# Performance work log

Hardware: AMD Instinct MI355X
Metric: run time of the kernel (lower is better)

## Reference

```python
import jax, jax.numpy as jnp
import numpy as np

E = 16   # stroke embedding dim
H = 2    # attention heads
HD = E // H

def setup_inputs() -> dict:
    key = jax.random.key(0)
    ks = jax.random.split(key, 16)
    N, L, B = 100000, 8, 200000
    node_features = jax.random.normal(ks[0], (N, 6), dtype=jnp.float32)
    stroke_to_loop = jax.random.randint(ks[1], (B, L), 0, N, dtype=jnp.int64)
    def lin(k, o, i):
        bound = 1.0 / np.sqrt(i)
        kw, kb = jax.random.split(k)
        w = jax.random.uniform(kw, (o, i), jnp.float32, -bound, bound)
        b = jax.random.uniform(kb, (o,), jnp.float32, -bound, bound)
        return w, b
    fc1_w, fc1_b = lin(ks[2], 32, 6)
    fc2_w, fc2_b = lin(ks[3], E, 32)
    in_proj_w, in_proj_b = lin(ks[4], 3 * E, E)
    out_proj_w, out_proj_b = lin(ks[5], E, E)
    fc_w, fc_b = lin(ks[6], 32, E)
    fco_w, fco_b = lin(ks[7], 32, 32)
    return {"node_features": node_features, "stroke_to_loop": stroke_to_loop,
            "fc1_w": fc1_w, "fc1_b": fc1_b, "fc2_w": fc2_w, "fc2_b": fc2_b,
            "in_proj_w": in_proj_w, "in_proj_b": in_proj_b,
            "out_proj_w": out_proj_w, "out_proj_b": out_proj_b,
            "fc_w": fc_w, "fc_b": fc_b, "fco_w": fco_w, "fco_b": fco_b}

def reference(node_features, stroke_to_loop, fc1_w, fc1_b, fc2_w, fc2_b,
              in_proj_w, in_proj_b, out_proj_w, out_proj_b,
              fc_w, fc_b, fco_w, fco_b):
    B, L = stroke_to_loop.shape
    # per-loop gather: [B, L, 6]
    strokes = node_features[stroke_to_loop]
    # stroke MLP: 6 -> 32 -> 16
    h = jax.nn.relu(jnp.einsum('bli,oi->blo', strokes, fc1_w) + fc1_b)
    x = jnp.einsum('bli,oi->blo', h, fc2_w) + fc2_b  # [B, L, E]
    # multihead self-attention (embed_dim=16, heads=2)
    qkv = jnp.einsum('ble,oe->blo', x, in_proj_w) + in_proj_b  # [B, L, 3E]
    q, k, v = jnp.split(qkv, 3, axis=-1)
    q = q.reshape(B, L, H, HD)
    k = k.reshape(B, L, H, HD)
    v = v.reshape(B, L, H, HD)
    scores = jnp.einsum('blhd,bmhd->bhlm', q, k) / np.sqrt(HD).astype(np.float32)
    attn = jax.nn.softmax(scores, axis=-1)
    ctx = jnp.einsum('bhlm,bmhd->blhd', attn, v).reshape(B, L, E)
    attn_out = jnp.einsum('ble,oe->blo', ctx, out_proj_w) + out_proj_b
    # fc -> relu -> mean over strokes -> fc_output
    y = jax.nn.relu(jnp.einsum('ble,oe->blo', attn_out, fc_w) + fc_b)
    y = y.mean(axis=1)  # [B, 32]
    return jnp.einsum('bi,oi->bo', y, fco_w) + fco_b
```

## Files before the change

kernel.cpp:

```cpp
#include <hip/hip_runtime.h>


typedef float f32x4 __attribute__((ext_vector_type(4)));
typedef __fp16 h2 __attribute__((ext_vector_type(2)));

static __device__ __forceinline__ unsigned h2u(h2 v) { return __builtin_bit_cast(unsigned, v); }
static __device__ __forceinline__ h2 u2h(unsigned v) { return __builtin_bit_cast(h2, v); }
static __device__ __forceinline__ h2 f2h(float v) { return __builtin_bit_cast(h2, v); }
static __device__ __forceinline__ float h2f(h2 v) { return __builtin_bit_cast(float, v); }
#define DPPH2(x, ctrl) u2h((unsigned)__builtin_amdgcn_update_dpp( \
    (int)h2u(x), (int)h2u(x), (ctrl), 0xF, 0xF, false))
#define SWZH(x, pat) u2h((unsigned)__builtin_amdgcn_ds_swizzle((int)h2u(x), (pat)))

#if defined(__has_builtin) && __has_builtin(__builtin_amdgcn_fdot2)
#define FDOT2(a, b, c) __builtin_amdgcn_fdot2((a), (b), (c), false)
#else
#define FDOT2(a, b, c) fmaf((float)(a).x, (float)(b).x, fmaf((float)(a).y, (float)(b).y, (c)))
#endif

#if defined(__has_builtin) && __has_builtin(__builtin_elementwise_fma)
#define PKFMA(a, b, c) __builtin_elementwise_fma((a), (b), (c))
#else
#define PKFMA(a, b, c) ((a) * (b) + (c))
#endif

__global__ __launch_bounds__(256) void prep_kernel(
    const float* __restrict__ nf,
    const float* __restrict__ w1, const float* __restrict__ b1,
    const float* __restrict__ w2, const float* __restrict__ b2,
    const float* __restrict__ wip, const float* __restrict__ bip,
    const float* __restrict__ fcw, const float* __restrict__ fcb,
    const float* __restrict__ opw, const float* __restrict__ opb,
    const float* __restrict__ fow,
    float* __restrict__ qkvt, h2* __restrict__ w3h,
    h2* __restrict__ fowh, float* __restrict__ b3, float* __restrict__ w3f,
    int N)
{
    if ((int)blockIdx.x == (int)gridDim.x - 1) {
        __shared__ float lw[512];
        int t = threadIdx.x;
#pragma unroll
        for (int rep = 0; rep < 2; ++rep) {
            int id = t + rep * 256;
            int o = id >> 4, j = id & 15;
            float acc = 0.f;
#pragma unroll
            for (int e = 0; e < 16; ++e)
                acc = fmaf(fcw[o * 16 + e], opw[e * 16 + j], acc);
            lw[id] = acc;
        }
        if (t < 32) {
            float bb = fcb[t];
#pragma unroll
            for (int e = 0; e < 16; ++e) bb = fmaf(fcw[t * 16 + e], opb[e], bb);
            b3[t] = bb;
        }
        fowh[t]       = __builtin_amdgcn_cvt_pkrtz(fow[2 * t],       fow[2 * t + 1]);
        fowh[t + 256] = __builtin_amdgcn_cvt_pkrtz(fow[2 * t + 512], fow[2 * t + 513]);
        __syncthreads();
        w3h[t] = __builtin_amdgcn_cvt_pkrtz(lw[2 * t], lw[2 * t + 1]);
        w3f[t] = lw[t];
        w3f[t + 256] = lw[t + 256];
        return;
    }
    int n = blockIdx.x * 256 + threadIdx.x;
    if (n >= N) return;
    const float2* nfp = reinterpret_cast<const float2*>(nf);
    float2 p0 = nfp[n * 3 + 0], p1 = nfp[n * 3 + 1], p2 = nfp[n * 3 + 2];
    float f[6] = {p0.x, p0.y, p1.x, p1.y, p2.x, p2.y};
    float h[32];
#pragma unroll
    for (int o = 0; o < 32; ++o) {
        float acc = b1[o];
#pragma unroll
        for (int i = 0; i < 6; ++i) acc = fmaf(f[i], w1[o * 6 + i], acc);
        h[o] = fmaxf(acc, 0.f);
    }
    float x[16];
#pragma unroll
    for (int e = 0; e < 16; ++e) {
        float acc = b2[e];
#pragma unroll
        for (int i = 0; i < 32; ++i) acc = fmaf(h[i], w2[e * 32 + i], acc);
        x[e] = acc;
    }
    float qkv[48];
#pragma unroll
    for (int c = 0; c < 48; ++c) {
        float acc = bip[c];
#pragma unroll
        for (int e = 0; e < 16; ++e) acc = fmaf(x[e], wip[c * 16 + e], acc);
        qkv[c] = acc;
    }
    const float cs = 0.35355339059327373f * 1.4426950408889634f;
#pragma unroll
    for (int c = 0; c < 16; ++c) qkv[c] *= cs;
    h2 ph[24];
#pragma unroll
    for (int i = 0; i < 24; ++i)
        ph[i] = __builtin_amdgcn_cvt_pkrtz(qkv[2 * i], qkv[2 * i + 1]);
    f32x4* dst = reinterpret_cast<f32x4*>(qkvt) + (size_t)n * 6;
#pragma unroll
    for (int t2 = 0; t2 < 6; ++t2) {
        f32x4 w;
        w.x = h2f(ph[4 * t2 + 0]); w.y = h2f(ph[4 * t2 + 1]);
        w.z = h2f(ph[4 * t2 + 2]); w.w = h2f(ph[4 * t2 + 3]);
        dst[t2] = w;
    }
}

__global__ __launch_bounds__(256) void attn_tail_kernel(
    const int* __restrict__ s2l, const float* __restrict__ qkvt,
    const h2* __restrict__ w3h, const float* __restrict__ b3,
    const h2* __restrict__ fowh, const float* __restrict__ fob,
    float* __restrict__ out, int B)
{
    int tid = blockIdx.x * 256 + threadIdx.x;
    int l = tid & 7;
    int g = tid >> 3;
    int npair = (B + 1) >> 1;
    if (g >= npair) return;
    int b0 = 2 * g, b1 = 2 * g + 1;
    bool have1 = (b1 < B);
    int idx0 = s2l[b0 * 8 + l];
    int idx1 = s2l[(have1 ? b1 : b0) * 8 + l];
    const f32x4* qp0 = reinterpret_cast<const f32x4*>(qkvt) + (size_t)idx0 * 6;
    const f32x4* qp1 = reinterpret_cast<const f32x4*>(qkvt) + (size_t)idx1 * 6;

    f32x4 x0 = qp0[0], x1 = qp0[1], x2 = qp0[2], x3 = qp0[3], x4 = qp0[4], x5 = qp0[5];
    f32x4 y0 = qp1[0], y1 = qp1[1], y2 = qp1[2], y3 = qp1[3], y4 = qp1[4], y5 = qp1[5];

    h2 qh[2][8], kh[2][8], vh[2][8];
    qh[0][0]=f2h(x0.x); qh[0][1]=f2h(x0.y); qh[0][2]=f2h(x0.z); qh[0][3]=f2h(x0.w);
    qh[0][4]=f2h(x1.x); qh[0][5]=f2h(x1.y); qh[0][6]=f2h(x1.z); qh[0][7]=f2h(x1.w);
    kh[0][0]=f2h(x2.x); kh[0][1]=f2h(x2.y); kh[0][2]=f2h(x2.z); kh[0][3]=f2h(x2.w);
    kh[0][4]=f2h(x3.x); kh[0][5]=f2h(x3.y); kh[0][6]=f2h(x3.z); kh[0][7]=f2h(x3.w);
    vh[0][0]=f2h(x4.x); vh[0][1]=f2h(x4.y); vh[0][2]=f2h(x4.z); vh[0][3]=f2h(x4.w);
    vh[0][4]=f2h(x5.x); vh[0][5]=f2h(x5.y); vh[0][6]=f2h(x5.z); vh[0][7]=f2h(x5.w);
    qh[1][0]=f2h(y0.x); qh[1][1]=f2h(y0.y); qh[1][2]=f2h(y0.z); qh[1][3]=f2h(y0.w);
    qh[1][4]=f2h(y1.x); qh[1][5]=f2h(y1.y); qh[1][6]=f2h(y1.z); qh[1][7]=f2h(y1.w);
    kh[1][0]=f2h(y2.x); kh[1][1]=f2h(y2.y); kh[1][2]=f2h(y2.z); kh[1][3]=f2h(y2.w);
    kh[1][4]=f2h(y3.x); kh[1][5]=f2h(y3.y); kh[1][6]=f2h(y3.z); kh[1][7]=f2h(y3.w);
    vh[1][0]=f2h(y4.x); vh[1][1]=f2h(y4.y); vh[1][2]=f2h(y4.z); vh[1][3]=f2h(y4.w);
    vh[1][4]=f2h(y5.x); vh[1][5]=f2h(y5.y); vh[1][6]=f2h(y5.z); vh[1][7]=f2h(y5.w);

    h2 k7[2][8];
#pragma unroll
    for (int d = 0; d < 8; ++d) {
        k7[0][d] = DPPH2(kh[0][d], 0x141);
        k7[1][d] = DPPH2(kh[1][d], 0x141);
    }

    float s0[2][8], s1[2][8];
#define SC_ID(i, slot, KS) { float u0 = 0.f, u1 = 0.f; \
    _Pragma("unroll") for (int d = 0; d < 4; ++d) { \
        u0 = FDOT2(qh[i][d], KS[i][d], u0); \
        u1 = FDOT2(qh[i][4 + d], KS[i][4 + d], u1); } \
    s0[i][slot] = u0; s1[i][slot] = u1; }
#define SC_DPP(i, slot, KS, CTRL) { float u0 = 0.f, u1 = 0.f; \
    _Pragma("unroll") for (int d = 0; d < 4; ++d) { \
        u0 = FDOT2(qh[i][d], DPPH2(KS[i][d], CTRL), u0); \
        u1 = FDOT2(qh[i][4 + d], DPPH2(KS[i][4 + d], CTRL), u1); } \
    s0[i][slot] = u0; s1[i][slot] = u1; }
    SC_ID(0, 0, kh)          SC_ID(1, 0, kh)
    SC_DPP(0, 1, kh, 0xB1)   SC_DPP(1, 1, kh, 0xB1)
    SC_DPP(0, 2, kh, 0x4E)   SC_DPP(1, 2, kh, 0x4E)
    SC_DPP(0, 3, kh, 0x1B)   SC_DPP(1, 3, kh, 0x1B)
    SC_DPP(0, 4, k7, 0x1B)   SC_DPP(1, 4, k7, 0x1B)
    SC_DPP(0, 5, k7, 0x4E)   SC_DPP(1, 5, k7, 0x4E)
    SC_DPP(0, 6, k7, 0xB1)   SC_DPP(1, 6, k7, 0xB1)
    SC_ID(0, 7, k7)          SC_ID(1, 7, k7)
#undef SC_ID
#undef SC_DPP

    h2 eA[2][8], eB[2][8];
#pragma unroll
    for (int i = 0; i < 2; ++i) {
        float e0[8], e1[8];
        float sum0 = 0.f, sum1 = 0.f;
#pragma unroll
        for (int m = 0; m < 8; ++m) {
            e0[m] = exp2f(s0[i][m]); sum0 += e0[m];
            e1[m] = exp2f(s1[i][m]); sum1 += e1[m];
        }
        float r0 = __builtin_amdgcn_rcpf(sum0);
        float r1 = __builtin_amdgcn_rcpf(sum1);
#pragma unroll
        for (int m = 0; m < 8; ++m) {
            float n0 = e0[m] * r0, n1 = e1[m] * r1;
            eA[i][m] = __builtin_amdgcn_cvt_pkrtz(n0, n0);
            eB[i][m] = __builtin_amdgcn_cvt_pkrtz(n1, n1);
        }
    }

    h2 v7[2][8];
#pragma unroll
    for (int d = 0; d < 8; ++d) {
        v7[0][d] = DPPH2(vh[0][d], 0x141);
        v7[1][d] = DPPH2(vh[1][d], 0x141);
    }

    h2 cx[2][8];
    h2 hz; hz.x = (__fp16)0.f; hz.y = (__fp16)0.f;
#pragma unroll
    for (int i = 0; i < 2; ++i)
#pragma unroll
        for (int d = 0; d < 8; ++d) cx[i][d] = hz;
#define CTX_ID(i, slot, VS) { \
    _Pragma("unroll") for (int d = 0; d < 4; ++d) { \
        cx[i][d]     = PKFMA(eA[i][slot], VS[i][d],     cx[i][d]); \
        cx[i][4 + d] = PKFMA(eB[i][slot], VS[i][4 + d], cx[i][4 + d]); } }
#define CTX_DPP(i, slot, VS, CTRL) { \
    _Pragma("unroll") for (int d = 0; d < 4; ++d) { \
        cx[i][d]     = PKFMA(eA[i][slot], DPPH2(VS[i][d], CTRL),     cx[i][d]); \
        cx[i][4 + d] = PKFMA(eB[i][slot], DPPH2(VS[i][4 + d], CTRL), cx[i][4 + d]); } }
    CTX_ID(0, 0, vh)          CTX_ID(1, 0, vh)
    CTX_DPP(0, 1, vh, 0xB1)   CTX_DPP(1, 1, vh, 0xB1)
    CTX_DPP(0, 2, vh, 0x4E)   CTX_DPP(1, 2, vh, 0x4E)
    CTX_DPP(0, 3, vh, 0x1B)   CTX_DPP(1, 3, vh, 0x1B)
    CTX_DPP(0, 4, v7, 0x1B)   CTX_DPP(1, 4, v7, 0x1B)
    CTX_DPP(0, 5, v7, 0x4E)   CTX_DPP(1, 5, v7, 0x4E)
    CTX_DPP(0, 6, v7, 0xB1)   CTX_DPP(1, 6, v7, 0xB1)
    CTX_ID(0, 7, v7)          CTX_ID(1, 7, v7)
#undef CTX_ID
#undef CTX_DPP

    h2 yh[2][16];
#pragma unroll
    for (int i = 0; i < 16; ++i) {
        float ba = b3[2 * i], bb = b3[2 * i + 1];
        float ya0 = ba, yb0 = bb, ya1 = ba, yb1 = bb;
#pragma unroll
        for (int jj = 0; jj < 8; ++jj) {
            h2 wa = w3h[(2 * i) * 8 + jj];
            h2 wb = w3h[(2 * i + 1) * 8 + jj];
            ya0 = FDOT2(cx[0][jj], wa, ya0);
            ya1 = FDOT2(cx[1][jj], wa, ya1);
            yb0 = FDOT2(cx[0][jj], wb, yb0);
            yb1 = FDOT2(cx[1][jj], wb, yb1);
        }
        yh[0][i] = __builtin_amdgcn_cvt_pkrtz(fmaxf(ya0, 0.f), fmaxf(yb0, 0.f));
        yh[1][i] = __builtin_amdgcn_cvt_pkrtz(fmaxf(ya1, 0.f), fmaxf(yb1, 0.f));
    }

#pragma unroll
    for (int i = 0; i < 16; ++i) {
#pragma unroll
        for (int j = 0; j < 2; ++j) {
            yh[j][i] = yh[j][i] + SWZH(yh[j][i], 0x041F);
            yh[j][i] = yh[j][i] + SWZH(yh[j][i], 0x081F);
            yh[j][i] = yh[j][i] + SWZH(yh[j][i], 0x101F);
        }
    }

    float o4a[4], o4b[4];
#pragma unroll
    for (int j = 0; j < 4; ++j) {
        int oo = l * 4 + j;
        float acc0 = 0.f, acc1 = 0.f;
#pragma unroll
        for (int i = 0; i < 16; ++i) {
            h2 w = fowh[oo * 16 + i];
            acc0 = FDOT2(yh[0][i], w, acc0);
            acc1 = FDOT2(yh[1][i], w, acc1);
        }
        float bo = fob[oo];
        o4a[j] = fmaf(acc0, 0.125f, bo);
        o4b[j] = fmaf(acc1, 0.125f, bo);
    }
    f32x4 res0; res0.x = o4a[0]; res0.y = o4a[1]; res0.z = o4a[2]; res0.w = o4a[3];
    __builtin_nontemporal_store(res0, reinterpret_cast<f32x4*>(out) + (b0 * 8 + l));
    if (have1) {
        f32x4 res1; res1.x = o4b[0]; res1.y = o4b[1]; res1.z = o4b[2]; res1.w = o4b[3];
        __builtin_nontemporal_store(res1, reinterpret_cast<f32x4*>(out) + (b1 * 8 + l));
    }
}

__global__ __launch_bounds__(256) void loop_embed_kernel(
    const float* __restrict__ nf, const int* __restrict__ s2l,
    const float* __restrict__ w1, const float* __restrict__ b1,
    const float* __restrict__ w2, const float* __restrict__ b2,
    const float* __restrict__ wip, const float* __restrict__ bip,
    const float* __restrict__ w3, const float* __restrict__ b3,
    const float* __restrict__ fow, const float* __restrict__ fob,
    float* __restrict__ out, int B)
{
    int tid = blockIdx.x * 256 + threadIdx.x;
    int b = tid >> 3;
    if (b >= B) return;
    int l = tid & 7;
    int idx = s2l[b * 8 + l];
    const float2* nfp = reinterpret_cast<const float2*>(nf);
    float2 p0 = nfp[idx * 3 + 0], p1 = nfp[idx * 3 + 1], p2 = nfp[idx * 3 + 2];
    float f[6] = {p0.x, p0.y, p1.x, p1.y, p2.x, p2.y};
    float h[32];
#pragma unroll
    for (int o = 0; o < 32; ++o) {
        float acc = b1[o];
#pragma unroll
        for (int i = 0; i < 6; ++i) acc = fmaf(f[i], w1[o * 6 + i], acc);
        h[o] = fmaxf(acc, 0.f);
    }
    float x[16];
#pragma unroll
    for (int e = 0; e < 16; ++e) {
        float acc = b2[e];
#pragma unroll
        for (int i = 0; i < 32; ++i) acc = fmaf(h[i], w2[e * 32 + i], acc);
        x[e] = acc;
    }
    float q[16], k[16], v[16];
#pragma unroll
    for (int c = 0; c < 16; ++c) {
        float aq = bip[c], ak = bip[16 + c], av = bip[32 + c];
#pragma unroll
        for (int e = 0; e < 16; ++e) {
            aq = fmaf(x[e], wip[c * 16 + e], aq);
            ak = fmaf(x[e], wip[(16 + c) * 16 + e], ak);
            av = fmaf(x[e], wip[(32 + c) * 16 + e], av);
        }
        q[c] = aq; k[c] = ak; v[c] = av;
    }
    int lane = threadIdx.x & 63;
    int gb = lane & 56;
    float s0[8], s1[8];
#pragma unroll
    for (int m = 0; m < 8; ++m) {
        float a0 = 0.f, a1 = 0.f;
#pragma unroll
        for (int d = 0; d < 8; ++d) {
            a0 = fmaf(q[d], __shfl(k[d], gb + m, 64), a0);
            a1 = fmaf(q[8 + d], __shfl(k[8 + d], gb + m, 64), a1);
        }
        s0[m] = a0; s1[m] = a1;
    }
    const float sc = 0.35355339059327373f;
    float mx0 = s0[0], mx1 = s1[0];
#pragma unroll
    for (int m = 1; m < 8; ++m) { mx0 = fmaxf(mx0, s0[m]); mx1 = fmaxf(mx1, s1[m]); }
    float e0[8], e1[8];
    float sum0 = 0.f, sum1 = 0.f;
#pragma unroll
    for (int m = 0; m < 8; ++m) {
        e0[m] = __expf((s0[m] - mx0) * sc); sum0 += e0[m];
        e1[m] = __expf((s1[m] - mx1) * sc); sum1 += e1[m];
    }
    float r0 = 1.0f / sum0, r1 = 1.0f / sum1;
    float ctx[16];
#pragma unroll
    for (int c = 0; c < 16; ++c) ctx[c] = 0.f;
#pragma unroll
    for (int m = 0; m < 8; ++m) {
#pragma unroll
        for (int c = 0; c < 8; ++c)
            ctx[c] = fmaf(e0[m], __shfl(v[c], gb + m, 64), ctx[c]);
#pragma unroll
        for (int c = 8; c < 16; ++c)
            ctx[c] = fmaf(e1[m], __shfl(v[c], gb + m, 64), ctx[c]);
    }
#pragma unroll
    for (int c = 0; c < 8; ++c)  ctx[c] *= r0;
#pragma unroll
    for (int c = 8; c < 16; ++c) ctx[c] *= r1;
    float y[32];
#pragma unroll
    for (int o = 0; o < 32; ++o) {
        float acc = b3[o];
#pragma unroll
        for (int j = 0; j < 16; ++j) acc = fmaf(ctx[j], w3[o * 16 + j], acc);
        y[o] = fmaxf(acc, 0.f);
    }
#pragma unroll
    for (int o = 0; o < 32; ++o) {
        y[o] += __shfl_xor(y[o], 1, 64);
        y[o] += __shfl_xor(y[o], 2, 64);
        y[o] += __shfl_xor(y[o], 4, 64);
    }
    float o4[4];
#pragma unroll
    for (int j = 0; j < 4; ++j) {
        int oo = l * 4 + j;
        float acc = 0.f;
#pragma unroll
        for (int i = 0; i < 32; ++i) acc = fmaf(y[i], fow[oo * 32 + i], acc);
        o4[j] = fmaf(acc, 0.125f, fob[oo]);
    }
    reinterpret_cast<float4*>(out)[b * 8 + l] = make_float4(o4[0], o4[1], o4[2], o4[3]);
}

extern "C" void kernel_launch(void* const* d_in, const int* in_sizes, int n_in,
                              void* d_out, int out_size, void* d_ws, size_t ws_size,
                              hipStream_t stream) {
    const float* nf  = (const float*)d_in[0];
    const int*   s2l = (const int*)d_in[1];
    const float* w1  = (const float*)d_in[2];
    const float* b1  = (const float*)d_in[3];
    const float* w2  = (const float*)d_in[4];
    const float* b2  = (const float*)d_in[5];
    const float* wip = (const float*)d_in[6];
    const float* bip = (const float*)d_in[7];
    const float* opw = (const float*)d_in[8];
    const float* opb = (const float*)d_in[9];
    const float* fcw = (const float*)d_in[10];
    const float* fcb = (const float*)d_in[11];
    const float* fow = (const float*)d_in[12];
    const float* fob = (const float*)d_in[13];
    float* out = (float*)d_out;

    int N = in_sizes[0] / 6;
    int B = in_sizes[1] / 8;

    unsigned* wsd = (unsigned*)d_ws;
    h2*    w3h  = (h2*)(wsd);
    h2*    fowh = (h2*)(wsd + 256);
    float* b3   = (float*)(wsd + 768);
    float* w3f  = (float*)(wsd + 800);
    float* qkvt = (float*)(wsd + 1312);

    size_t need = (size_t)(1312 + (size_t)N * 12) * 4;

    if (ws_size >= need) {
        int NB = (N + 255) / 256;
        prep_kernel<<<NB + 1, 256, 0, stream>>>(
            nf, w1, b1, w2, b2, wip, bip, fcw, fcb, opw, opb, fow,
            qkvt, w3h, fowh, b3, w3f, N);
        int npair = (B + 1) >> 1;
        int threads = npair * 8;
        int blocks = (threads + 255) / 256;
        attn_tail_kernel<<<blocks, 256, 0, stream>>>(
            s2l, qkvt, w3h, b3, fowh, fob, out, B);
    } else {
        prep_kernel<<<1, 256, 0, stream>>>(
            nf, w1, b1, w2, b2, wip, bip, fcw, fcb, opw, opb, fow,
            qkvt, w3h, fowh, b3, w3f, 0);
        int blocks = (B * 8 + 255) / 256;
        loop_embed_kernel<<<blocks, 256, 0, stream>>>(
            nf, s2l, w1, b1, w2, b2, wip, bip, w3f, b3, fow, fob, out, B);
    }
    (void)n_in; (void)out_size;
}
```

Measured before the change: 83.07 us.

## Fuse prep and attention kernels into one cooperative persistent kernel with grid sync

Combines the per-node QKV precompute and the per-loop attention tail into one cooperative kernel. It uses grid-stride loops sized to occupancy and a grid-wide barrier between the two phases. This is meant to remove the second kernel launch and the gap between the kernels. In exchange it adds a grid sync and host-side occupancy queries on every call, and it gives up the larger oversubscribed grid. The old two-kernel path is kept as a fallback if the cooperative launch fails.

```diff
diff --git a/kernel.cpp b/kernel.cpp
--- a/kernel.cpp
+++ b/kernel.cpp
@@ -1,5 +1,8 @@
 #include <hip/hip_runtime.h>
-
+#include <hip/hip_cooperative_groups.h>
+
+
+namespace cg = cooperative_groups;
 
 typedef float f32x4 __attribute__((ext_vector_type(4)));
 typedef __fp16 h2 __attribute__((ext_vector_type(2)));
@@ -24,47 +27,14 @@
 #define PKFMA(a, b, c) ((a) * (b) + (c))
 #endif
 
-__global__ __launch_bounds__(256) void prep_kernel(
+
+static __device__ __forceinline__ void qkv_node_body(
     const float* __restrict__ nf,
     const float* __restrict__ w1, const float* __restrict__ b1,
     const float* __restrict__ w2, const float* __restrict__ b2,
     const float* __restrict__ wip, const float* __restrict__ bip,
-    const float* __restrict__ fcw, const float* __restrict__ fcb,
-    const float* __restrict__ opw, const float* __restrict__ opb,
-    const float* __restrict__ fow,
-    float* __restrict__ qkvt, h2* __restrict__ w3h,
-    h2* __restrict__ fowh, float* __restrict__ b3, float* __restrict__ w3f,
-    int N)
+    float* __restrict__ qkvt, int n)
 {
-    if ((int)blockIdx.x == (int)gridDim.x - 1) {
-        __shared__ float lw[512];
-        int t = threadIdx.x;
-#pragma unroll
-        for (int rep = 0; rep < 2; ++rep) {
-            int id = t + rep * 256;
-            int o = id >> 4, j = id & 15;
-            float acc = 0.f;
-#pragma unroll
-            for (int e = 0; e < 16; ++e)
-                acc = fmaf(fcw[o * 16 + e], opw[e * 16 + j], acc);
-            lw[id] = acc;
-        }
-        if (t < 32) {
-            float bb = fcb[t];
-#pragma unroll
-            for (int e = 0; e < 16; ++e) bb = fmaf(fcw[t * 16 + e], opb[e], bb);
-            b3[t] = bb;
-        }
-        fowh[t]       = __builtin_amdgcn_cvt_pkrtz(fow[2 * t],       fow[2 * t + 1]);
-        fowh[t + 256] = __builtin_amdgcn_cvt_pkrtz(fow[2 * t + 512], fow[2 * t + 513]);
-        __syncthreads();
-        w3h[t] = __builtin_amdgcn_cvt_pkrtz(lw[2 * t], lw[2 * t + 1]);
-        w3f[t] = lw[t];
-        w3f[t + 256] = lw[t + 256];
-        return;
-    }
-    int n = blockIdx.x * 256 + threadIdx.x;
-    if (n >= N) return;
     const float2* nfp = reinterpret_cast<const float2*>(nf);
     float2 p0 = nfp[n * 3 + 0], p1 = nfp[n * 3 + 1], p2 = nfp[n * 3 + 2];
     float f[6] = {p0.x, p0.y, p1.x, p1.y, p2.x, p2.y};
@@ -109,17 +79,14 @@
     }
 }
 
-__global__ __launch_bounds__(256) void attn_tail_kernel(
+static __device__ __forceinline__ void attn_pair_body(
     const int* __restrict__ s2l, const float* __restrict__ qkvt,
     const h2* __restrict__ w3h, const float* __restrict__ b3,
     const h2* __restrict__ fowh, const float* __restrict__ fob,
-    float* __restrict__ out, int B)
+    float* __restrict__ out, int B, int t)
 {
-    int tid = blockIdx.x * 256 + threadIdx.x;
-    int l = tid & 7;
-    int g = tid >> 3;
-    int npair = (B + 1) >> 1;
-    if (g >= npair) return;
+    int l = t & 7;
+    int g = t >> 3;
     int b0 = 2 * g, b1 = 2 * g + 1;
     bool have1 = (b1 < B);
     int idx0 = s2l[b0 * 8 + l];
@@ -276,6 +243,110 @@
     }
 }
 
+__global__ __launch_bounds__(256) void fused_kernel(
+    const float* __restrict__ nf,
+    const float* __restrict__ w1, const float* __restrict__ b1,
+    const float* __restrict__ w2, const float* __restrict__ b2,
+    const float* __restrict__ wip, const float* __restrict__ bip,
+    const float* __restrict__ fcw, const float* __restrict__ fcb,
+    const float* __restrict__ opw, const float* __restrict__ opb,
+    const float* __restrict__ fow, const float* __restrict__ fob,
+    const int* __restrict__ s2l,
+    float* __restrict__ qkvt, h2* __restrict__ w3h,
+    h2* __restrict__ fowh, float* __restrict__ b3w,
+    float* __restrict__ out, int N, int B)
+{
+    int t = threadIdx.x;
+    if (blockIdx.x == 0) {
+        __shared__ float lw[512];
+#pragma unroll
+        for (int rep = 0; rep < 2; ++rep) {
+            int id = t + rep * 256;
+            int o = id >> 4, j = id & 15;
+            float acc = 0.f;
+#pragma unroll
+            for (int e = 0; e < 16; ++e)
+                acc = fmaf(fcw[o * 16 + e], opw[e * 16 + j], acc);
+            lw[id] = acc;
+        }
+        if (t < 32) {
+            float bb = fcb[t];
+#pragma unroll
+            for (int e = 0; e < 16; ++e) bb = fmaf(fcw[t * 16 + e], opb[e], bb);
+            b3w[t] = bb;
+        }
+        fowh[t]       = __builtin_amdgcn_cvt_pkrtz(fow[2 * t],       fow[2 * t + 1]);
+        fowh[t + 256] = __builtin_amdgcn_cvt_pkrtz(fow[2 * t + 512], fow[2 * t + 513]);
+        __syncthreads();
+        w3h[t] = __builtin_amdgcn_cvt_pkrtz(lw[2 * t], lw[2 * t + 1]);
+    }
+    for (int n = blockIdx.x * 256 + t; n < N; n += gridDim.x * 256)
+        qkv_node_body(nf, w1, b1, w2, b2, wip, bip, qkvt, n);
+
+    cg::this_grid().sync();
+
+    int npair = (B + 1) >> 1;
+    int total = npair * 8;
+    for (int i = blockIdx.x * 256 + t; i < total; i += gridDim.x * 256)
+        attn_pair_body(s2l, qkvt, w3h, b3w, fowh, fob, out, B, i);
+}
+
+__global__ __launch_bounds__(256) void prep_kernel(
+    const float* __restrict__ nf,
+    const float* __restrict__ w1, const float* __restrict__ b1,
+    const float* __restrict__ w2, const float* __restrict__ b2,
+    const float* __restrict__ wip, const float* __restrict__ bip,
+    const float* __restrict__ fcw, const float* __restrict__ fcb,
+    const float* __restrict__ opw, const float* __restrict__ opb,
+    const float* __restrict__ fow,
+    float* __restrict__ qkvt, h2* __restrict__ w3h,
+    h2* __restrict__ fowh, float* __restrict__ b3, float* __restrict__ w3f,
+    int N)
+{
+    if ((int)blockIdx.x == (int)gridDim.x - 1) {
+        __shared__ float lw[512];
+        int t = threadIdx.x;
+#pragma unroll
+        for (int rep = 0; rep < 2; ++rep) {
+            int id = t + rep * 256;
+            int o = id >> 4, j = id & 15;
+            float acc = 0.f;
+#pragma unroll
+            for (int e = 0; e < 16; ++e)
+                acc = fmaf(fcw[o * 16 + e], opw[e * 16 + j], acc);
+            lw[id] = acc;
+        }
+        if (t < 32) {
+            float bb = fcb[t];
+#pragma unroll
+            for (int e = 0; e < 16; ++e) bb = fmaf(fcw[t * 16 + e], opb[e], bb);
+            b3[t] = bb;
+        }
+        fowh[t]       = __builtin_amdgcn_cvt_pkrtz(fow[2 * t],       fow[2 * t + 1]);
+        fowh[t + 256] = __builtin_amdgcn_cvt_pkrtz(fow[2 * t + 512], fow[2 * t + 513]);
+        __syncthreads();
+        w3h[t] = __builtin_amdgcn_cvt_pkrtz(lw[2 * t], lw[2 * t + 1]);
+        w3f[t] = lw[t];
+        w3f[t + 256] = lw[t + 256];
+        return;
+    }
+    int n = blockIdx.x * 256 + threadIdx.x;
+    if (n >= N) return;
+    qkv_node_body(nf, w1, b1, w2, b2, wip, bip, qkvt, n);
+}
+
+__global__ __launch_bounds__(256) void attn_tail_kernel(
+    const int* __restrict__ s2l, const float* __restrict__ qkvt,
+    const h2* __restrict__ w3h, const float* __restrict__ b3,
+    const h2* __restrict__ fowh, const float* __restrict__ fob,
+    float* __restrict__ out, int B)
+{
+    int tid = blockIdx.x * 256 + threadIdx.x;
+    int npair = (B + 1) >> 1;
+    if ((tid >> 3) >= npair) return;
+    attn_pair_body(s2l, qkvt, w3h, b3, fowh, fob, out, B, tid);
+}
+
 __global__ __launch_bounds__(256) void loop_embed_kernel(
     const float* __restrict__ nf, const int* __restrict__ s2l,
     const float* __restrict__ w1, const float* __restrict__ b1,
@@ -420,15 +491,42 @@
     size_t need = (size_t)(1312 + (size_t)N * 12) * 4;
 
     if (ws_size >= need) {
-        int NB = (N + 255) / 256;
-        prep_kernel<<<NB + 1, 256, 0, stream>>>(
-            nf, w1, b1, w2, b2, wip, bip, fcw, fcb, opw, opb, fow,
-            qkvt, w3h, fowh, b3, w3f, N);
-        int npair = (B + 1) >> 1;
-        int threads = npair * 8;
-        int blocks = (threads + 255) / 256;
-        attn_tail_kernel<<<blocks, 256, 0, stream>>>(
-            s2l, qkvt, w3h, b3, fowh, fob, out, B);
+        bool done = false;
+        int dev = 0;
+        if (hipGetDevice(&dev) == hipSuccess) {
+            int numCU = 0, bpc = 0;
+            if (hipDeviceGetAttribute(&numCU, hipDeviceAttributeMultiprocessorCount,
+                                      dev) == hipSuccess && numCU > 0 &&
+                hipOccupancyMaxActiveBlocksPerMultiprocessor(
+                    &bpc, fused_kernel, 256, 0) == hipSuccess && bpc > 0) {
+                int grid = numCU * bpc;
+                int npair = (B + 1) >> 1;
+                int needB = (npair * 8 + 255) / 256;
+                int needN = (N + 255) / 256;
+                int mx = needB > needN ? needB : needN;
+                if (grid > mx) grid = mx;
+                if (grid < 1) grid = 1;
+                void* kargs[] = {
+                    (void*)&nf, (void*)&w1, (void*)&b1, (void*)&w2, (void*)&b2,
+                    (void*)&wip, (void*)&bip, (void*)&fcw, (void*)&fcb,
+                    (void*)&opw, (void*)&opb, (void*)&fow, (void*)&fob,
+                    (void*)&s2l, (void*)&qkvt, (void*)&w3h, (void*)&fowh,
+                    (void*)&b3, (void*)&out, (void*)&N, (void*)&B};
+                if (hipLaunchCooperativeKernel(fused_kernel, dim3(grid), dim3(256),
+                                               kargs, 0, stream) == hipSuccess)
+                    done = true;
+            }
+        }
+        if (!done) {
+            int NB = (N + 255) / 256;
+            prep_kernel<<<NB + 1, 256, 0, stream>>>(
+                nf, w1, b1, w2, b2, wip, bip, fcw, fcb, opw, opb, fow,
+                qkvt, w3h, fowh, b3, w3f, N);
+            int npair = (B + 1) >> 1;
+            int blocks = (npair * 8 + 255) / 256;
+            attn_tail_kernel<<<blocks, 256, 0, stream>>>(
+                s2l, qkvt, w3h, b3, fowh, fob, out, B);
+        }
     } else {
         prep_kernel<<<1, 256, 0, stream>>>(
             nf, w1, b1, w2, b2, wip, bip, fcw, fcb, opw, opb, fow,
```

Measured after the change: 84.35 us. Within noise of the previous version (+1.5%).
